# Optimization experiments

Hardware: AMD Instinct MI355X
Metric: run time of the kernel (lower is better)

The kernel has to match this reference:

```python
import jax, jax.numpy as jnp
import numpy as np

N_HEAD = 4
D_K = 512 // N_HEAD  # 128
PAD = 5  # (kernel 11 - 1) // 2, sanm_shift=0 -> symmetric 'same' padding
EPS = 1e-5


def layer_norm(x, w, b):
    m = jnp.mean(x, axis=-1, keepdims=True)
    v = jnp.mean(jnp.square(x - m), axis=-1, keepdims=True)
    return (x - m) * jax.lax.rsqrt(v + EPS) * w + b


def setup_inputs() -> dict:
    key = jax.random.key(0)
    ks = jax.random.split(key, 8)
    B, T, D = 64, 218, 512
    s = 0.05
    return {
        "x": jax.random.normal(ks[0], (B, T, D), jnp.float32),
        "masks": jnp.ones((B, T), jnp.float32),
        "ln0_w": jax.random.uniform(ks[1], (D,), jnp.float32, 0.9, 1.1),
        "ln0_b": jnp.zeros((D,), jnp.float32),
        "ln1_w": jax.random.uniform(ks[2], (D,), jnp.float32, 0.9, 1.1),
        "ln1_b": jnp.zeros((D,), jnp.float32),
        "qkv_w": jax.random.normal(ks[3], (D, 3 * D), jnp.float32) * s,
        "qkv_b": jnp.zeros((3 * D,), jnp.float32),
        "out_w": jax.random.normal(ks[4], (D, D), jnp.float32) * s,
        "out_b": jnp.zeros((D,), jnp.float32),
        "fsmn_w": jax.random.normal(ks[5], (D, D, 11), jnp.float32) * s,
        "w1": jax.random.normal(ks[6], (D, 4 * D), jnp.float32) * s,
        "b1": jnp.zeros((4 * D,), jnp.float32),
        "w2": jax.random.normal(ks[7], (4 * D, D), jnp.float32) * s,
        "b2": jnp.zeros((D,), jnp.float32),
    }


def encoder_layer(x, masks, ln0_w, ln0_b, ln1_w, ln1_b, qkv_w, qkv_b,
                  out_w, out_b, fsmn_w, w1, b1, w2, b2):
    B, T, D = x.shape
    m = masks[..., None]  # (B,T,1)

    # ---- self_attn_sanm block ----
    residual = x
    h = layer_norm(x, ln0_w, ln0_b)
    qkv = h @ qkv_w + qkv_b                      # (B,T,3D)
    q, k, v = jnp.split(qkv, 3, axis=-1)         # each (B,T,D)

    # FSMN memory branch on (masked) v: Conv1d(512,512,11), 'same' padding
    vm = v * m
    # torch conv weight (out,in,k) -> jax 'WIO' kernel (k,in,out)
    kern = jnp.transpose(fsmn_w, (2, 1, 0))
    fsmn = jax.lax.conv_general_dilated(
        vm, kern, window_strides=(1,), padding=[(PAD, PAD)],
        dimension_numbers=("NWC", "WIO", "NWC"))
    fsmn = (fsmn + vm) * m                       # (B,T,D)

    # multi-head attention
    def heads(t):  # (B,T,D) -> (B,H,T,dk)
        return t.reshape(B, T, N_HEAD, D_K).transpose(0, 2, 1, 3)
    qh, kh, vh = heads(q), heads(k), heads(v)
    scores = jnp.einsum("bhqd,bhkd->bhqk", qh, kh) / np.sqrt(D_K)
    neg = jnp.finfo(scores.dtype).min
    scores = jnp.where(masks[:, None, None, :] > 0, scores, neg)
    attn = jax.nn.softmax(scores, axis=-1)
    ctx = jnp.einsum("bhqk,bhkd->bhqd", attn, vh)
    ctx = ctx.transpose(0, 2, 1, 3).reshape(B, T, D)
    att_out = ctx @ out_w + out_b + fsmn
    x = residual + att_out

    # ---- feed-forward block (512 -> 2048 -> 512, relu) ----
    residual = x
    h = layer_norm(x, ln1_w, ln1_b)
    ffn = jax.nn.relu(h @ w1 + b1) @ w2 + b2
    return residual + ffn


def reference(x, masks, ln0_w, ln0_b, ln1_w, ln1_b, qkv_w, qkv_b,
              out_w, out_b, fsmn_w, w1, b1, w2, b2):
    return encoder_layer(x, masks, ln0_w, ln0_b, ln1_w, ln1_b,
                         qkv_w, qkv_b, out_w, out_b, fsmn_w, w1, b1, w2, b2)
```

## Files before the change

### kernel.cpp

```cpp
#include <hip/hip_runtime.h>
#include <cstdint>

#define B_   64
#define T_   218
#define TP_  228
#define D_   512
#define M_   13952
#define MT_  109
#define H_   4
#define DK_  128
#define N3_  1536
#define DFF_ 2048
#define KC_  5632

typedef unsigned short u16;
using short8 = __attribute__((ext_vector_type(8))) short;
using f32x4  = __attribute__((ext_vector_type(4))) float;

__device__ __forceinline__ float b2f(u16 u) {
  union { float f; uint32_t i; } v; v.i = ((uint32_t)u) << 16; return v.f;
}
__device__ __forceinline__ u16 f2b(float f) {
  union { float f; uint32_t i; } v; v.f = f;
  uint32_t r = v.i + 0x7fffu + ((v.i >> 16) & 1u);
  return (u16)(r >> 16);
}
union U8 { uint4 v; u16 u[8]; };

__device__ __forceinline__ void gll16(const u16* g, u16* l) {
  __builtin_amdgcn_global_load_lds(
      (const __attribute__((address_space(1))) unsigned int*)g,
      (__attribute__((address_space(3))) unsigned int*)l, 16, 0, 0);
}


template<int MODE>
__global__ __launch_bounds__(256, 2)
void gemm_u(const u16* __restrict__ A, int sA, const u16* __restrict__ Bt, int sB,
            const float* __restrict__ bias, const u16* __restrict__ convb,
            u16* __restrict__ vmout,
            const float* __restrict__ add_f, void* __restrict__ outp,
            int N, int K, int ntc, const float* __restrict__ masks)
{
  __shared__ u16 As[128 * 32];
  __shared__ u16 Bs[128 * 32];

  const int xcd = blockIdx.x & 7;
  const int lin = blockIdx.x >> 3;
  const int nt = lin % ntc;
  const int mt = xcd + 8 * (lin / ntc);
  if (mt >= MT_) return;
  const int m0 = mt * 128, n0 = nt * 128;

  const int tid = threadIdx.x, lane = tid & 63, w = tid >> 6;
  const int wm = (w >> 1) * 64, wn = (w & 1) * 64;
  const int l15 = lane & 15, qd = lane >> 4;

  const int rl = lane >> 2;
  const int ce = ((lane & 3) ^ ((lane >> 3) & 3)) * 8;
  const int sw8 = (qd ^ ((lane >> 1) & 3)) * 8;
  const int r0 = m0 + w * 16 + rl, r1 = r0 + 64;
  const u16* ag0 = A + (size_t)r0 * sA + ce;
  const u16* ag1 = A + (size_t)r1 * sA + ce;
  const u16* bg0 = Bt + (size_t)(n0 + w * 16 + rl) * sB + ce;
  const u16* bg1 = bg0 + (size_t)64 * sB;
  u16* lA0 = As + w * 512;
  u16* lA1 = As + 2048 + w * 512;
  u16* lB0 = Bs + w * 512;
  u16* lB1 = Bs + 2048 + w * 512;

  const f32x4 z4 = {0.f, 0.f, 0.f, 0.f};
  f32x4 acc[4][4];
#pragma unroll
  for (int i = 0; i < 4; i++)
#pragma unroll
    for (int j = 0; j < 4; j++) acc[i][j] = z4;

  for (int k0 = 0; k0 < K; k0 += 32) {
    __syncthreads();
    gll16(ag0 + k0, lA0);
    gll16(ag1 + k0, lA1);
    gll16(bg0 + k0, lB0);
    gll16(bg1 + k0, lB1);
    __syncthreads();
    short8 af[4], bf[4];
#pragma unroll
    for (int mi = 0; mi < 4; mi++) af[mi] = *(const short8*)&As[(wm + mi * 16 + l15) * 32 + sw8];
#pragma unroll
    for (int ni = 0; ni < 4; ni++) bf[ni] = *(const short8*)&Bs[(wn + ni * 16 + l15) * 32 + sw8];
#pragma unroll
    for (int mi = 0; mi < 4; mi++)
#pragma unroll
      for (int ni = 0; ni < 4; ni++)
        acc[mi][ni] = __builtin_amdgcn_mfma_f32_16x16x32_bf16(af[mi], bf[ni], acc[mi][ni], 0, 0, 0);
  }

#pragma unroll
  for (int ni = 0; ni < 4; ni++) {
    const int c = n0 + wn + ni * 16 + l15;
    const float bv = bias[c];
#pragma unroll
    for (int mi = 0; mi < 4; mi++) {
#pragma unroll
      for (int rg = 0; rg < 4; rg++) {
        const int r = m0 + wm + mi * 16 + qd * 4 + rg;
        float v = acc[mi][ni][rg] + bv;
        if (MODE == 0) {
          ((u16*)outp)[(size_t)r * N + c] = f2b(v);
          if (c >= 1024) {
            const int b = r / T_, t = r - b * T_;
            vmout[((size_t)b * TP_ + t + 5) * D_ + (c - 1024)] = f2b(v * masks[r]);
          }
        } else if (MODE == 1) {
          const size_t idx = (size_t)r * N + c;
          ((float*)outp)[idx] = v + b2f(convb[idx]) + add_f[idx];
        } else if (MODE == 2) {
          ((u16*)outp)[(size_t)r * N + c] = f2b(fmaxf(v, 0.f));
        } else {
          const size_t idx = (size_t)r * N + c;
          ((float*)outp)[idx] = v + add_f[idx];
        }
      }
    }
  }
}

__global__ __launch_bounds__(512, 2)
void conv_gemm(const u16* __restrict__ vmpad, const u16* __restrict__ Wt,
               const float* __restrict__ masks, u16* __restrict__ convb)
{
  __shared__ u16 smem[2][30208];

  const int nt = blockIdx.x & 7, b = blockIdx.x >> 3;
  const int n0 = nt * 64;
  const int base = b * TP_;

  const int tid = threadIdx.x, lane = tid & 63, w = tid >> 6;
  const int wm = (w >> 2) * 112, wn = (w & 3) * 16;
  const int l15 = lane & 15, qd = lane >> 4;
  const int rl = lane >> 2;
  const int ce = ((lane & 3) ^ ((lane >> 3) & 3)) * 8;

  int abase[7];
#pragma unroll
  for (int mi = 0; mi < 7; mi++) abase[mi] = (wm + mi * 16 + l15) * 64;
  int toff[11];
#pragma unroll
  for (int tap = 0; tap < 11; tap++)
    toff[tap] = tap * 64 + ((qd ^ (((l15 + tap) >> 1) & 3)) << 4);
  const int swb8 = (qd ^ ((l15 >> 1) & 3)) * 8;

  const f32x4 z4 = {0.f, 0.f, 0.f, 0.f};
  f32x4 acc[7];
#pragma unroll
  for (int i = 0; i < 7; i++) acc[i] = z4;

#define STAGE(kc, bufi)                                                        \
  {                                                                            \
    const int kb = (kc) * 32;                                                  \
    u16* Ab_ = smem[bufi];                                                     \
    u16* Bb_ = smem[bufi] + 7680;                                              \
    for (int c = w; c < 15; c += 8)                                            \
      gll16(vmpad + (size_t)(base + c * 16 + rl) * D_ + kb + ce, Ab_ + c * 512);\
    for (int c = w; c < 44; c += 8) {                                          \
      const int tap_ = c >> 2, q_ = c & 3;                                     \
      gll16(Wt + (size_t)(n0 + q_ * 16 + rl) * KC_ + tap_ * 512 + kb + ce,     \
            Bb_ + c * 512);                                                    \
    }                                                                          \
  }

  STAGE(0, 0);
  __syncthreads();

  for (int kc = 0; kc < 16; kc++) {
    const int cur = kc & 1;
    if (kc < 15) STAGE(kc + 1, cur ^ 1);
    const char* Ab = (const char*)smem[cur];
    const u16* Bb = smem[cur] + 7680;
#pragma unroll
    for (int tap = 0; tap < 11; tap++) {
      short8 bf = *(const short8*)&Bb[tap * 2048 + (wn + l15) * 32 + swb8];
#pragma unroll
      for (int mi = 0; mi < 7; mi++) {
        short8 af = *(const short8*)(Ab + (abase[mi] + toff[tap]));
        acc[mi] = __builtin_amdgcn_mfma_f32_16x16x32_bf16(af, bf, acc[mi], 0, 0, 0);
      }
    }
    __syncthreads();
  }
#undef STAGE

#pragma unroll
  for (int mi = 0; mi < 7; mi++) {
#pragma unroll
    for (int rg = 0; rg < 4; rg++) {
      const int rlcl = wm + mi * 16 + qd * 4 + rg;
      if (rlcl < T_) {
        const int r = b * T_ + rlcl;
        const int vrow = base + rlcl + 5;
        const float m = masks[r];
        const int c = n0 + wn + l15;
        const float vm = b2f(vmpad[(size_t)vrow * D_ + c]);
        convb[(size_t)r * D_ + c] = f2b((acc[mi][rg] + vm) * m);
      }
    }
  }
}

__global__ __launch_bounds__(256, 2)
void attn_fused(const u16* __restrict__ qkv, const float* __restrict__ masks,
                u16* __restrict__ ctx)
{
  __shared__ u16 smem[29696];
  __shared__ float red0[4][64];
  __shared__ float red1[4][64];
  u16* Qs = smem;
  u16* Ks = smem + 64 * 136;
  u16* Ps = smem;
  u16* Vs = smem + 64 * 232;

  const int tid = threadIdx.x, lane = tid & 63, w = tid >> 6;
  const int l15 = lane & 15, qd = lane >> 4;
  const int bh = blockIdx.y, b = bh >> 2, h = bh & 3;
  const int q0 = blockIdx.x * 64;
  const uint4 uz = make_uint4(0, 0, 0, 0);

#pragma unroll
  for (int i = 0; i < 4; i++) {
    const int ch = tid + i * 256;
    const int row = ch >> 4, cg = (ch & 15) * 8;
    const int t = q0 + row;
    uint4 v = uz;
    if (t < T_) v = *(const uint4*)(qkv + ((size_t)b * T_ + t) * N3_ + h * DK_ + cg);
    *(uint4*)&Qs[row * 136 + cg] = v;
  }

  const f32x4 z4 = {0.f, 0.f, 0.f, 0.f};
  f32x4 acc[4][4];
#pragma unroll
  for (int i = 0; i < 4; i++)
#pragma unroll
    for (int j = 0; j < 4; j++) acc[i][j] = z4;

#pragma unroll
  for (int kc = 0; kc < 4; kc++) {
    __syncthreads();
#pragma unroll
    for (int i = 0; i < 4; i++) {
      const int ch = tid + i * 256;
      const int row = ch >> 4, cg = (ch & 15) * 8;
      const int t = kc * 64 + row;
      uint4 v = uz;
      if (t < T_) v = *(const uint4*)(qkv + ((size_t)b * T_ + t) * N3_ + D_ + h * DK_ + cg);
      *(uint4*)&Ks[row * 136 + cg] = v;
    }
    __syncthreads();
#pragma unroll
    for (int ks = 0; ks < 4; ks++) {
      short8 bf = *(const short8*)&Ks[(w * 16 + l15) * 136 + ks * 32 + qd * 8];
#pragma unroll
      for (int mi = 0; mi < 4; mi++) {
        short8 af = *(const short8*)&Qs[(mi * 16 + l15) * 136 + ks * 32 + qd * 8];
        acc[kc][mi] = __builtin_amdgcn_mfma_f32_16x16x32_bf16(af, bf, acc[kc][mi], 0, 0, 0);
      }
    }
  }

  const float scale = 0.08838834764831845f;
  const int colb = w * 16 + l15;
  bool valid[4];
#pragma unroll
  for (int kc = 0; kc < 4; kc++) {
    const int col = kc * 64 + colb;
    valid[kc] = (col < T_) && (masks[b * T_ + col] > 0.f);
  }

  float mx[4][4];
#pragma unroll
  for (int mi = 0; mi < 4; mi++)
#pragma unroll
    for (int rg = 0; rg < 4; rg++) {
      float m = -1e30f;
#pragma unroll
      for (int kc = 0; kc < 4; kc++)
        if (valid[kc]) m = fmaxf(m, acc[kc][mi][rg] * scale);
      for (int d = 1; d < 16; d <<= 1) m = fmaxf(m, __shfl_xor(m, d, 64));
      mx[mi][rg] = m;
    }
  if (l15 == 0) {
#pragma unroll
    for (int mi = 0; mi < 4; mi++)
#pragma unroll
      for (int rg = 0; rg < 4; rg++) red0[w][mi * 16 + qd * 4 + rg] = mx[mi][rg];
  }
  __syncthreads();
#pragma unroll
  for (int mi = 0; mi < 4; mi++)
#pragma unroll
    for (int rg = 0; rg < 4; rg++) {
      const int r = mi * 16 + qd * 4 + rg;
      mx[mi][rg] = fmaxf(fmaxf(red0[0][r], red0[1][r]), fmaxf(red0[2][r], red0[3][r]));
    }
  float sm[4][4];
#pragma unroll
  for (int mi = 0; mi < 4; mi++)
#pragma unroll
    for (int rg = 0; rg < 4; rg++) {
      float s = 0.f;
#pragma unroll
      for (int kc = 0; kc < 4; kc++)
        if (valid[kc]) s += __expf(acc[kc][mi][rg] * scale - mx[mi][rg]);
      for (int d = 1; d < 16; d <<= 1) s += __shfl_xor(s, d, 64);
      sm[mi][rg] = s;
    }
  if (l15 == 0) {
#pragma unroll
    for (int mi = 0; mi < 4; mi++)
#pragma unroll
      for (int rg = 0; rg < 4; rg++) red1[w][mi * 16 + qd * 4 + rg] = sm[mi][rg];
  }
  __syncthreads();
#pragma unroll
  for (int mi = 0; mi < 4; mi++)
#pragma unroll
    for (int rg = 0; rg < 4; rg++) {
      const int r = mi * 16 + qd * 4 + rg;
      const float inv = 1.f / (red1[0][r] + red1[1][r] + red1[2][r] + red1[3][r]);
#pragma unroll
      for (int kc = 0; kc < 4; kc++) {
        const int col = kc * 64 + colb;
        if (col < 224) {
          const float p = valid[kc] ? __expf(acc[kc][mi][rg] * scale - mx[mi][rg]) * inv : 0.f;
          Ps[r * 232 + col] = f2b(p);
        }
      }
    }

  const int kvg = tid >> 4, dg = tid & 15;
#pragma unroll
  for (int half = 0; half < 2; ++half) {
    __syncthreads();
#pragma unroll
    for (int r = 0; r < 14; ++r) {
      const int kv = r * 16 + kvg;
      ushort4 vv = make_ushort4(0, 0, 0, 0);
      if (kv < T_)
        vv = *(const ushort4*)(qkv + ((size_t)b * T_ + kv) * N3_ + 1024 + h * DK_ + half * 64 + dg * 4);
      Vs[(dg * 4 + 0) * 232 + kv] = vv.x;
      Vs[(dg * 4 + 1) * 232 + kv] = vv.y;
      Vs[(dg * 4 + 2) * 232 + kv] = vv.z;
      Vs[(dg * 4 + 3) * 232 + kv] = vv.w;
    }
    __syncthreads();
    f32x4 a2[4] = {z4, z4, z4, z4};
#pragma unroll
    for (int k0 = 0; k0 < 7; ++k0) {
      short8 af = *(const short8*)&Ps[(w * 16 + l15) * 232 + k0 * 32 + qd * 8];
#pragma unroll
      for (int nt = 0; nt < 4; ++nt) {
        short8 bf = *(const short8*)&Vs[(nt * 16 + l15) * 232 + k0 * 32 + qd * 8];
        a2[nt] = __builtin_amdgcn_mfma_f32_16x16x32_bf16(af, bf, a2[nt], 0, 0, 0);
      }
    }
    const int tb = q0 + w * 16 + qd * 4;
#pragma unroll
    for (int nt = 0; nt < 4; ++nt) {
      const int d = h * DK_ + half * 64 + nt * 16 + l15;
#pragma unroll
      for (int rg = 0; rg < 4; ++rg) {
        const int tt = tb + rg;
        if (tt < T_) ctx[((size_t)b * T_ + tt) * D_ + d] = f2b(a2[nt][rg]);
      }
    }
  }
}

__global__ __launch_bounds__(256)
void ln_k(const float* __restrict__ x, const float* __restrict__ wgt,
          const float* __restrict__ bia, u16* __restrict__ outp)
{
  const int lane = threadIdx.x & 63, wv = threadIdx.x >> 6;
  const size_t row = (size_t)blockIdx.x * 4 + wv;
  const float* rp = x + row * D_ + lane * 8;
  float v[8], s = 0.f, s2 = 0.f;
  float4 r0 = *(const float4*)rp;
  float4 r1 = *(const float4*)(rp + 4);
  v[0] = r0.x; v[1] = r0.y; v[2] = r0.z; v[3] = r0.w;
  v[4] = r1.x; v[5] = r1.y; v[6] = r1.z; v[7] = r1.w;
#pragma unroll
  for (int i = 0; i < 8; i++) { s += v[i]; s2 += v[i] * v[i]; }
  for (int d = 1; d < 64; d <<= 1) { s += __shfl_xor(s, d, 64); s2 += __shfl_xor(s2, d, 64); }
  const float mean = s * (1.f / 512.f);
  const float var  = s2 * (1.f / 512.f) - mean * mean;
  const float rs   = rsqrtf(var + 1e-5f);
  float4 w0 = *(const float4*)(wgt + lane * 8);
  float4 w1 = *(const float4*)(wgt + lane * 8 + 4);
  float4 b0 = *(const float4*)(bia + lane * 8);
  float4 b1 = *(const float4*)(bia + lane * 8 + 4);
  const float wv8[8] = {w0.x, w0.y, w0.z, w0.w, w1.x, w1.y, w1.z, w1.w};
  const float bv8[8] = {b0.x, b0.y, b0.z, b0.w, b1.x, b1.y, b1.z, b1.w};
  U8 o;
#pragma unroll
  for (int i = 0; i < 8; i++)
    o.u[i] = f2b((v[i] - mean) * rs * wv8[i] + bv8[i]);
  *(uint4*)(outp + row * D_ + lane * 8) = o.v;
}

__global__ __launch_bounds__(256)
void prep_all(const float* __restrict__ qkv_w, const float* __restrict__ out_w,
              const float* __restrict__ w1, const float* __restrict__ w2,
              const float* __restrict__ fsmn_w,
              u16* __restrict__ qkv_wT, u16* __restrict__ out_wT,
              u16* __restrict__ w1T, u16* __restrict__ w2T,
              u16* __restrict__ fsmnW2, u16* __restrict__ vmpad)
{
  const int bid = blockIdx.x;
  if (bid < 3072) {
    const float* src; u16* dst; int K, N, tb;
    if (bid < 768)       { src = qkv_w; dst = qkv_wT; K = 512;  N = 1536; tb = bid; }
    else if (bid < 1024) { src = out_w; dst = out_wT; K = 512;  N = 512;  tb = bid - 768; }
    else if (bid < 2048) { src = w1;    dst = w1T;    K = 512;  N = 2048; tb = bid - 1024; }
    else                 { src = w2;    dst = w2T;    K = 2048; N = 512;  tb = bid - 2048; }
    const int ktiles = K / 32;
    const int k0 = (tb % ktiles) * 32, n0 = (tb / ktiles) * 32;
    __shared__ float tile[32][33];
    const int x = threadIdx.x & 31, y = threadIdx.x >> 5;
#pragma unroll
    for (int j = 0; j < 4; j++)
      tile[y + j * 8][x] = src[(size_t)(k0 + y + j * 8) * N + n0 + x];
    __syncthreads();
#pragma unroll
    for (int j = 0; j < 4; j++)
      dst[(size_t)(n0 + y + j * 8) * K + k0 + x] = f2b(tile[x][y + j * 8]);
  } else if (bid < 4096) {
    const int idx = (bid - 3072) * 256 + threadIdx.x;
    const int o = idx >> 9, i = idx & 511;
    const float* s = fsmn_w + (size_t)idx * 11;
#pragma unroll
    for (int tap = 0; tap < 11; ++tap)
      fsmnW2[(size_t)o * KC_ + tap * 512 + i] = f2b(s[tap]);
  } else {
    const int e8 = (bid - 4096) * 256 + threadIdx.x;
    const int e  = e8 * 8;
    const int c  = e & 511;
    const int pr = e >> 9;
    int row;
    if (pr < 640) {
      const int b = pr / 10, j = pr % 10;
      row = b * TP_ + ((j < 5) ? j : (218 + j));
    } else {
      row = B_ * TP_ + (pr - 640);
    }
    *(uint4*)(vmpad + (size_t)row * D_ + c) = make_uint4(0, 0, 0, 0);
  }
}

extern "C" void kernel_launch(void* const* d_in, const int* in_sizes, int n_in,
                              void* d_out, int out_size, void* d_ws, size_t ws_size,
                              hipStream_t stream)
{
  const float* x      = (const float*)d_in[0];
  const float* masks  = (const float*)d_in[1];
  const float* ln0_w  = (const float*)d_in[2];
  const float* ln0_b  = (const float*)d_in[3];
  const float* ln1_w  = (const float*)d_in[4];
  const float* ln1_b  = (const float*)d_in[5];
  const float* qkv_w  = (const float*)d_in[6];
  const float* qkv_b  = (const float*)d_in[7];
  const float* out_w  = (const float*)d_in[8];
  const float* out_b  = (const float*)d_in[9];
  const float* fsmn_w = (const float*)d_in[10];
  const float* w1     = (const float*)d_in[11];
  const float* b1     = (const float*)d_in[12];
  const float* w2     = (const float*)d_in[13];
  const float* b2     = (const float*)d_in[14];
  float* outp = (float*)d_out;
  u16* ws   = (u16*)d_ws;

  size_t off = 0;
  u16* qkv_wT = ws + off; off += (size_t)1536 * 512;
  u16* out_wT = ws + off; off += (size_t)512 * 512;
  u16* w1T    = ws + off; off += (size_t)2048 * 512;
  u16* w2T    = ws + off; off += (size_t)512 * 2048;
  u16* fsmnW2 = ws + off; off += (size_t)512 * KC_;
  u16* slotA  = ws + off; off += (size_t)M_ * 512;
  u16* qkvb   = ws + off; off += (size_t)M_ * 1536;
  u16* vmpad  = ws + off; off += (size_t)(B_ * TP_ + 320) * 512;
  u16* regionX= ws + off;
  u16* convb  = regionX;
  u16* hid    = regionX;
  u16* h1     = qkvb;
  float* x1   = (float*)(qkvb + (size_t)M_ * 512);

  prep_all<<<4126, 256, 0, stream>>>(qkv_w, out_w, w1, w2, fsmn_w,
                                     qkv_wT, out_wT, w1T, w2T, fsmnW2, vmpad);
  ln_k<<<M_ / 4, 256, 0, stream>>>(x, ln0_w, ln0_b, slotA);
  gemm_u<0><<<8 * 14 * 12, 256, 0, stream>>>(
      slotA, 512, qkv_wT, 512, qkv_b, nullptr, vmpad, nullptr, qkvb,
      1536, 512, 12, masks);
  conv_gemm<<<512, 512, 0, stream>>>(vmpad, fsmnW2, masks, convb);
  attn_fused<<<dim3(4, 256), 256, 0, stream>>>(qkvb, masks, slotA);
  gemm_u<1><<<8 * 14 * 4, 256, 0, stream>>>(
      slotA, 512, out_wT, 512, out_b, convb, nullptr, x, x1,
      512, 512, 4, masks);
  ln_k<<<M_ / 4, 256, 0, stream>>>(x1, ln1_w, ln1_b, h1);
  gemm_u<2><<<8 * 14 * 16, 256, 0, stream>>>(
      h1, 512, w1T, 512, b1, nullptr, nullptr, nullptr, hid,
      2048, 512, 16, nullptr);
  gemm_u<3><<<8 * 14 * 4, 256, 0, stream>>>(
      hid, 2048, w2T, 2048, b2, nullptr, nullptr, x1, outp,
      512, 2048, 4, nullptr);
}
```

Before: 468.7 us.

## Process two batches per conv_gemm block to reuse FSMN weight tiles

The FSMN conv GEMM now has each block cover two batch sequences instead of one, and each wave computes two 16-column N subtiles. Every staged weight tile is reused across twice as many rows, which halves weight traffic from global memory and halves the grid to 256 blocks. The cost is more shared memory per block (about 151KB double-buffered), a larger accumulator footprint, and fewer blocks, which lowers occupancy and parallelism on a 256-CU device.

```diff
diff --git a/kernel.cpp b/kernel.cpp
--- a/kernel.cpp
+++ b/kernel.cpp
@@ -129,43 +129,48 @@
 void conv_gemm(const u16* __restrict__ vmpad, const u16* __restrict__ Wt,
                const float* __restrict__ masks, u16* __restrict__ convb)
 {
-  __shared__ u16 smem[2][30208];
-
-  const int nt = blockIdx.x & 7, b = blockIdx.x >> 3;
+  __shared__ u16 smem[2][37888];
+
+  const int nt = blockIdx.x & 7, qp = blockIdx.x >> 3;
   const int n0 = nt * 64;
-  const int base = b * TP_;
+  const int base = qp * 2 * TP_;
 
   const int tid = threadIdx.x, lane = tid & 63, w = tid >> 6;
-  const int wm = (w >> 2) * 112, wn = (w & 3) * 16;
+  const int qm = w >> 1;
+  const int wn = (w & 1) * 32;
+  const int wm = qm * 112;
+  const int lb = qm >> 1;
   const int l15 = lane & 15, qd = lane >> 4;
   const int rl = lane >> 2;
   const int ce = ((lane & 3) ^ ((lane >> 3) & 3)) * 8;
 
   int abase[7];
 #pragma unroll
-  for (int mi = 0; mi < 7; mi++) abase[mi] = (wm + mi * 16 + l15) * 64;
+  for (int mi = 0; mi < 7; mi++) abase[mi] = (wm + mi * 16 + l15 + 4 * lb) * 64;
   int toff[11];
 #pragma unroll
   for (int tap = 0; tap < 11; tap++)
-    toff[tap] = tap * 64 + ((qd ^ (((l15 + tap) >> 1) & 3)) << 4);
+    toff[tap] = tap * 64 + ((qd ^ (((l15 + 4 * lb + tap) >> 1) & 3)) << 4);
   const int swb8 = (qd ^ ((l15 >> 1) & 3)) * 8;
 
   const f32x4 z4 = {0.f, 0.f, 0.f, 0.f};
-  f32x4 acc[7];
-#pragma unroll
-  for (int i = 0; i < 7; i++) acc[i] = z4;
+  f32x4 acc[7][2];
+#pragma unroll
+  for (int i = 0; i < 7; i++) { acc[i][0] = z4; acc[i][1] = z4; }
 
 #define STAGE(kc, bufi)                                                        \
   {                                                                            \
     const int kb = (kc) * 32;                                                  \
     u16* Ab_ = smem[bufi];                                                     \
-    u16* Bb_ = smem[bufi] + 7680;                                              \
-    for (int c = w; c < 15; c += 8)                                            \
-      gll16(vmpad + (size_t)(base + c * 16 + rl) * D_ + kb + ce, Ab_ + c * 512);\
-    for (int c = w; c < 44; c += 8) {                                          \
-      const int tap_ = c >> 2, q_ = c & 3;                                     \
-      gll16(Wt + (size_t)(n0 + q_ * 16 + rl) * KC_ + tap_ * 512 + kb + ce,     \
-            Bb_ + c * 512);                                                    \
+    u16* Bb_ = smem[bufi] + 15360;                                             \
+    for (int c = w; c < 74; c += 8) {                                          \
+      if (c < 30) {                                                            \
+        gll16(vmpad + (size_t)(base + c * 16 + rl) * D_ + kb + ce, Ab_ + c * 512);\
+      } else {                                                                 \
+        const int cb_ = c - 30, tap_ = cb_ >> 2, q_ = cb_ & 3;                 \
+        gll16(Wt + (size_t)(n0 + q_ * 16 + rl) * KC_ + tap_ * 512 + kb + ce,   \
+              Bb_ + cb_ * 512);                                                \
+      }                                                                        \
     }                                                                          \
   }
 
@@ -176,14 +181,16 @@
     const int cur = kc & 1;
     if (kc < 15) STAGE(kc + 1, cur ^ 1);
     const char* Ab = (const char*)smem[cur];
-    const u16* Bb = smem[cur] + 7680;
+    const u16* Bb = smem[cur] + 15360;
 #pragma unroll
     for (int tap = 0; tap < 11; tap++) {
-      short8 bf = *(const short8*)&Bb[tap * 2048 + (wn + l15) * 32 + swb8];
+      short8 bf0 = *(const short8*)&Bb[tap * 2048 + (wn + l15) * 32 + swb8];
+      short8 bf1 = *(const short8*)&Bb[tap * 2048 + (wn + 16 + l15) * 32 + swb8];
 #pragma unroll
       for (int mi = 0; mi < 7; mi++) {
         short8 af = *(const short8*)(Ab + (abase[mi] + toff[tap]));
-        acc[mi] = __builtin_amdgcn_mfma_f32_16x16x32_bf16(af, bf, acc[mi], 0, 0, 0);
+        acc[mi][0] = __builtin_amdgcn_mfma_f32_16x16x32_bf16(af, bf0, acc[mi][0], 0, 0, 0);
+        acc[mi][1] = __builtin_amdgcn_mfma_f32_16x16x32_bf16(af, bf1, acc[mi][1], 0, 0, 0);
       }
     }
     __syncthreads();
@@ -194,14 +201,18 @@
   for (int mi = 0; mi < 7; mi++) {
 #pragma unroll
     for (int rg = 0; rg < 4; rg++) {
-      const int rlcl = wm + mi * 16 + qd * 4 + rg;
-      if (rlcl < T_) {
-        const int r = b * T_ + rlcl;
-        const int vrow = base + rlcl + 5;
+      const int row = wm + mi * 16 + qd * 4 + rg;
+      const int t = row - lb * 224;
+      if (t < T_) {
+        const int r = (qp * 2 + lb) * T_ + t;
+        const int vrow = base + lb * 228 + t + 5;
         const float m = masks[r];
-        const int c = n0 + wn + l15;
-        const float vm = b2f(vmpad[(size_t)vrow * D_ + c]);
-        convb[(size_t)r * D_ + c] = f2b((acc[mi][rg] + vm) * m);
+#pragma unroll
+        for (int ni = 0; ni < 2; ni++) {
+          const int c = n0 + wn + ni * 16 + l15;
+          const float vm = b2f(vmpad[(size_t)vrow * D_ + c]);
+          convb[(size_t)r * D_ + c] = f2b((acc[mi][ni][rg] + vm) * m);
+        }
       }
     }
   }
@@ -498,7 +509,7 @@
   gemm_u<0><<<8 * 14 * 12, 256, 0, stream>>>(
       slotA, 512, qkv_wT, 512, qkv_b, nullptr, vmpad, nullptr, qkvb,
       1536, 512, 12, masks);
-  conv_gemm<<<512, 512, 0, stream>>>(vmpad, fsmnW2, masks, convb);
+  conv_gemm<<<256, 512, 0, stream>>>(vmpad, fsmnW2, masks, convb);
   attn_fused<<<dim3(4, 256), 256, 0, stream>>>(qkvb, masks, slotA);
   gemm_u<1><<<8 * 14 * 4, 256, 0, stream>>>(
       slotA, 512, out_wT, 512, out_b, convb, nullptr, x, x1,
```

Result: faster. 446.5 us (-4.7%).
